# Performance work log

Measured on AMD Instinct MI355X. Metric: run time of the kernel, lower is better.

Reference implementation:

```python
import jax, jax.numpy as jnp
import numpy as np

# --- architecture constants (match HashTriEmbedder defaults) ---
L = 16               # n_levels
F = 2                # n_features_per_level
LOG2_T = 19
T = 2 ** LOG2_T      # hashmap size per table
BASE, FINEST = 16.0, 512.0
GROWTH = np.exp((np.log(FINEST) - np.log(BASE)) / (L - 1))
RES = np.floor(BASE * GROWTH ** np.arange(L)).astype(np.float32)   # [L] per-level resolution
BOX_MIN = np.zeros(3, np.float32)
BOX_MAX = np.ones(3, np.float32)
# corner offset order matches bilinear_interp: 0=(0,0), 1=(0,1), 2=(1,0), 3=(1,1)
OFFSETS = np.array([[0, 0], [0, 1], [1, 0], [1, 1]], np.int32)      # [4,2]
PLANE_AXES = [(0, 1), (0, 2), (1, 2)]                               # xy, xz, yz
PRIME = np.uint32(2654435761)
NPTS = 1048576


def hash2(coords):
    """Spatial hash of 2D integer coords -> int32 index in [0, T). coords: int32 [...,2]."""
    cu = coords.astype(jnp.uint32)
    h = cu[..., 0] ^ (cu[..., 1] * PRIME)
    return (h & jnp.uint32(T - 1)).astype(jnp.int32)


def setup_inputs() -> dict:
    key = jax.random.key(0)
    k1, k2 = jax.random.split(key)
    x = jax.random.uniform(k1, (NPTS, 3), jnp.float32)               # points in unit box
    # embeddings init: uniform(-1e-4, 1e-4); layout [plane, level, table, feat]
    emb = (jax.random.uniform(k2, (3, L, T, F), jnp.float32) * 2.0 - 1.0) * 1e-4
    return {"x": x, "emb": emb}


def _encode(x, emb):
    res = jnp.asarray(RES)                                           # [L]
    offs = jnp.asarray(OFFSETS)                                      # [4,2]
    outs = []
    for p, (a0, a1) in enumerate(PLANE_AXES):
        xp = x[:, jnp.array([a0, a1])]                               # [B,2] plane coords
        bmin = jnp.asarray(BOX_MIN[[a0, a1]])
        bmax = jnp.asarray(BOX_MAX[[a0, a1]])
        grid = (bmax - bmin)[None, :] / res[:, None]                 # [L,2] cell size per level
        t = (xp[None, :, :] - bmin) / grid[:, None, :]               # [L,B,2]
        bl = jnp.floor(t).astype(jnp.int32)                          # [L,B,2] bottom-left cell
        vmin = bl.astype(jnp.float32) * grid[:, None, :] + bmin      # [L,B,2] voxel min vertex
        w = (xp[None, :, :] - vmin) / grid[:, None, :]               # [L,B,2] interp weights
        corners = bl[:, :, None, :] + offs[None, None, :, :]         # [L,B,4,2]
        idx = hash2(corners)                                         # [L,B,4]
        # gather per-level tables: emb[p] is [L,T,F]
        ve = jax.vmap(lambda tab, i: tab[i])(emb[p], idx)            # [L,B,4,F]
        w0 = w[..., 0:1]
        w1 = w[..., 1:2]
        c0 = ve[:, :, 0] * (1.0 - w0) + ve[:, :, 2] * w0             # [L,B,F]
        c1 = ve[:, :, 1] * (1.0 - w0) + ve[:, :, 3] * w0
        outs.append(c0 * (1.0 - w1) + c1 * w1)                       # [L,B,F]
    # output ordering: for each level i, planes xy,xz,yz -> [B, L*3*F]
    stacked = jnp.stack(outs, axis=0)                                # [3,L,B,F]
    return stacked.transpose(2, 1, 0, 3).reshape(x.shape[0], L * 3 * F)


def reference(x, emb):
    return _encode(x, emb)
```

## Files before the change

kernel.cpp:

```cpp
#include <hip/hip_runtime.h>

#define HL 16
#define TBITS 19
#define TMASK ((1u << TBITS) - 1u)
#define HPRIME 2654435761u

__constant__ float c_g[HL] = {
    1.0f / 16.0f,  1.0f / 20.0f,  1.0f / 25.0f,  1.0f / 32.0f,
    1.0f / 40.0f,  1.0f / 50.0f,  1.0f / 64.0f,  1.0f / 80.0f,
    1.0f / 101.0f, 1.0f / 128.0f, 1.0f / 161.0f, 1.0f / 203.0f,
    1.0f / 256.0f, 1.0f / 322.0f, 1.0f / 406.0f, 1.0f / 512.0f};

__global__ __launch_bounds__(256) void hash_tri_kernel(
    const float* __restrict__ x, const float* __restrict__ emb,
    float* __restrict__ out, int npts) {
  int tid = blockIdx.x * 256 + threadIdx.x;
  int n = tid >> 4;
  int l = tid & 15;
  if (n >= npts) return;

  float g = c_g[l];
  const float* xp = x + (size_t)n * 3;
  float xv0 = xp[0], xv1 = xp[1], xv2 = xp[2];

  const float2* tabL = (const float2*)emb + ((size_t)l << TBITS);

  float w0s[3], w1s[3];
  unsigned off[12];

#pragma unroll
  for (int p = 0; p < 3; ++p) {
    float xa = (p == 2) ? xv1 : xv0;
    float xb = (p == 0) ? xv1 : xv2;

    float t0 = xa / g;
    float t1 = xb / g;
    float f0 = floorf(t0);
    float f1 = floorf(t1);
    int b0 = (int)f0;
    int b1 = (int)f1;
    float vm0 = f0 * g;
    float vm1 = f1 * g;
    w0s[p] = (xa - vm0) / g;
    w1s[p] = (xb - vm1) / g;

    unsigned k0 = (unsigned)b1 * HPRIME;
    unsigned k1 = k0 + HPRIME;
    unsigned u0 = (unsigned)b0;
    unsigned u1 = u0 + 1u;

    unsigned pbase = (unsigned)(p * HL) << TBITS;
    off[p * 4 + 0] = pbase + ((u0 ^ k0) & TMASK);
    off[p * 4 + 1] = pbase + ((u0 ^ k1) & TMASK);
    off[p * 4 + 2] = pbase + ((u1 ^ k0) & TMASK);
    off[p * 4 + 3] = pbase + ((u1 ^ k1) & TMASK);
  }

  float2 v[12];
#pragma unroll
  for (int i = 0; i < 12; ++i) v[i] = tabL[off[i]];

  float2* ob = (float2*)(out + (size_t)n * 96 + l * 6);
#pragma unroll
  for (int p = 0; p < 3; ++p) {
    float w0 = w0s[p], w1 = w1s[p];
    float om0 = 1.0f - w0;
    float om1 = 1.0f - w1;
    float2 v00 = v[p * 4 + 0], v01 = v[p * 4 + 1];
    float2 v10 = v[p * 4 + 2], v11 = v[p * 4 + 3];
    float c0x = v00.x * om0 + v10.x * w0;
    float c0y = v00.y * om0 + v10.y * w0;
    float c1x = v01.x * om0 + v11.x * w0;
    float c1y = v01.y * om0 + v11.y * w0;
    float2 r;
    r.x = c0x * om1 + c1x * w1;
    r.y = c0y * om1 + c1y * w1;
    ob[p] = r;
  }
}

extern "C" void kernel_launch(void* const* d_in, const int* in_sizes, int n_in,
                              void* d_out, int out_size, void* d_ws,
                              size_t ws_size, hipStream_t stream) {
  const float* x = (const float*)d_in[0];
  const float* emb = (const float*)d_in[1];
  float* out = (float*)d_out;
  int npts = in_sizes[0] / 3;
  int total = npts * 16;
  int blocks = (total + 255) / 256;
  hash_tri_kernel<<<blocks, 256, 0, stream>>>(x, emb, out, npts);
}
```

Before: 1.248 ms.

## Pair adjacent hash corners into float4 loads and stage output through LDS

When the cell's x coordinate is even, the two x-neighbour corners hash to adjacent table slots (index XOR 1), so each pair is fetched with one 16-byte load instead of two 8-byte gathers. Results are staged in shared memory and written out as coalesced float4 stores instead of scattered float2 writes. This adds a divergent branch per plane, a block-wide barrier and LDS traffic, and moves the gathers inside the per-plane loop, which may reduce how many loads are in flight at once.

Result: faster. 1.080 ms (-13.5%).

```diff
diff --git a/kernel.cpp b/kernel.cpp
--- a/kernel.cpp
+++ b/kernel.cpp
@@ -14,68 +14,90 @@
 __global__ __launch_bounds__(256) void hash_tri_kernel(
     const float* __restrict__ x, const float* __restrict__ emb,
     float* __restrict__ out, int npts) {
+  __shared__ float s_out[16 * 96];
+
   int tid = blockIdx.x * 256 + threadIdx.x;
   int n = tid >> 4;
   int l = tid & 15;
-  if (n >= npts) return;
+  int ln = threadIdx.x >> 4;
 
-  float g = c_g[l];
-  const float* xp = x + (size_t)n * 3;
-  float xv0 = xp[0], xv1 = xp[1], xv2 = xp[2];
+  if (n < npts) {
+    float g = c_g[l];
+    const float* xp = x + (size_t)n * 3;
+    float xv0 = xp[0], xv1 = xp[1], xv2 = xp[2];
 
-  const float2* tabL = (const float2*)emb + ((size_t)l << TBITS);
-
-  float w0s[3], w1s[3];
-  unsigned off[12];
+    const float2* tabL = (const float2*)emb + ((size_t)l << TBITS);
 
 #pragma unroll
-  for (int p = 0; p < 3; ++p) {
-    float xa = (p == 2) ? xv1 : xv0;
-    float xb = (p == 0) ? xv1 : xv2;
+    for (int p = 0; p < 3; ++p) {
+      float xa = (p == 2) ? xv1 : xv0;
+      float xb = (p == 0) ? xv1 : xv2;
 
-    float t0 = xa / g;
-    float t1 = xb / g;
-    float f0 = floorf(t0);
-    float f1 = floorf(t1);
-    int b0 = (int)f0;
-    int b1 = (int)f1;
-    float vm0 = f0 * g;
-    float vm1 = f1 * g;
-    w0s[p] = (xa - vm0) / g;
-    w1s[p] = (xb - vm1) / g;
+      float t0 = xa / g;
+      float t1 = xb / g;
+      float f0 = floorf(t0);
+      float f1 = floorf(t1);
+      int b0 = (int)f0;
+      int b1 = (int)f1;
+      float w0 = (xa - f0 * g) / g;
+      float w1 = (xb - f1 * g) / g;
 
-    unsigned k0 = (unsigned)b1 * HPRIME;
-    unsigned k1 = k0 + HPRIME;
-    unsigned u0 = (unsigned)b0;
-    unsigned u1 = u0 + 1u;
+      unsigned k0 = (unsigned)b1 * HPRIME;
+      unsigned k1 = k0 + HPRIME;
+      unsigned u0 = (unsigned)b0;
+      unsigned i00 = (u0 ^ k0) & TMASK;
+      unsigned i01 = (u0 ^ k1) & TMASK;
 
-    unsigned pbase = (unsigned)(p * HL) << TBITS;
-    off[p * 4 + 0] = pbase + ((u0 ^ k0) & TMASK);
-    off[p * 4 + 1] = pbase + ((u0 ^ k1) & TMASK);
-    off[p * 4 + 2] = pbase + ((u1 ^ k0) & TMASK);
-    off[p * 4 + 3] = pbase + ((u1 ^ k1) & TMASK);
+      const float2* tab = tabL + (((size_t)p * HL) << TBITS);
+      float2 v00, v01, v10, v11;
+      if ((u0 & 1u) == 0u) {
+        const float4* t4 = (const float4*)tab;
+        float4 a = t4[i00 >> 1];
+        float4 b = t4[i01 >> 1];
+        if (i00 & 1u) {
+          v00 = make_float2(a.z, a.w);
+          v10 = make_float2(a.x, a.y);
+        } else {
+          v00 = make_float2(a.x, a.y);
+          v10 = make_float2(a.z, a.w);
+        }
+        if (i01 & 1u) {
+          v01 = make_float2(b.z, b.w);
+          v11 = make_float2(b.x, b.y);
+        } else {
+          v01 = make_float2(b.x, b.y);
+          v11 = make_float2(b.z, b.w);
+        }
+      } else {
+        unsigned u1 = u0 + 1u;
+        v00 = tab[i00];
+        v01 = tab[i01];
+        v10 = tab[(u1 ^ k0) & TMASK];
+        v11 = tab[(u1 ^ k1) & TMASK];
+      }
+
+      float om0 = 1.0f - w0;
+      float om1 = 1.0f - w1;
+      float c0x = v00.x * om0 + v10.x * w0;
+      float c0y = v00.y * om0 + v10.y * w0;
+      float c1x = v01.x * om0 + v11.x * w0;
+      float c1y = v01.y * om0 + v11.y * w0;
+      int sb = ln * 96 + l * 6 + p * 2;
+      s_out[sb + 0] = c0x * om1 + c1x * w1;
+      s_out[sb + 1] = c0y * om1 + c1y * w1;
+    }
   }
+  __syncthreads();
 
-  float2 v[12];
-#pragma unroll
-  for (int i = 0; i < 12; ++i) v[i] = tabL[off[i]];
-
-  float2* ob = (float2*)(out + (size_t)n * 96 + l * 6);
-#pragma unroll
-  for (int p = 0; p < 3; ++p) {
-    float w0 = w0s[p], w1 = w1s[p];
-    float om0 = 1.0f - w0;
-    float om1 = 1.0f - w1;
-    float2 v00 = v[p * 4 + 0], v01 = v[p * 4 + 1];
-    float2 v10 = v[p * 4 + 2], v11 = v[p * 4 + 3];
-    float c0x = v00.x * om0 + v10.x * w0;
-    float c0y = v00.y * om0 + v10.y * w0;
-    float c1x = v01.x * om0 + v11.x * w0;
-    float c1y = v01.y * om0 + v11.y * w0;
-    float2 r;
-    r.x = c0x * om1 + c1x * w1;
-    r.y = c0y * om1 + c1y * w1;
-    ob[p] = r;
+  const float4* sf4 = (const float4*)s_out;
+  float4* of4 = (float4*)out;
+  size_t nf4 = (size_t)npts * 24;
+  size_t gbase = (size_t)blockIdx.x * 384;
+  size_t g0 = gbase + threadIdx.x;
+  if (g0 < nf4) of4[g0] = sf4[threadIdx.x];
+  if (threadIdx.x < 128) {
+    size_t g1 = gbase + 256 + threadIdx.x;
+    if (g1 < nf4) of4[g1] = sf4[256 + threadIdx.x];
   }
 }
 
```
